# Kernel tuning notes

Measured on AMD Instinct MI355X. Metric: run time of the kernel, lower is better.

## Reference

```python
import jax, jax.numpy as jnp
import numpy as np
from jax.scipy.special import logsumexp

DIM_RHO = 128
DIM_C = 128
HID_F = 512   # hidden of MLP2 f
HID_F2 = 256  # hidden of MLP f2 (fixed 128->256->128 in source)
B, S, N = 64, 2048, 100000


def setup_inputs() -> dict:
    key = jax.random.key(0)
    ks = jax.random.split(key, 16)
    def lin(k, fan_in, fan_out):
        bound = 1.0 / np.sqrt(fan_in)
        kw, kb = jax.random.split(k)
        W = jax.random.uniform(kw, (fan_in, fan_out), jnp.float32, -bound, bound)
        b = jax.random.uniform(kb, (fan_out,), jnp.float32, -bound, bound)
        return W, b
    rho = jax.random.normal(ks[0], (B, S, DIM_RHO), jnp.float32)
    c = jax.random.normal(ks[1], (N, DIM_C), jnp.float32)
    w = jax.random.uniform(ks[2], (B, S), jnp.float32, 0.1, 1.0)
    l = jax.random.uniform(ks[3], (B,), jnp.float32, 0.1, 1.0)
    roads = jax.random.randint(ks[4], (B, S), 0, N + 1)  # 0 = pad row
    f2_W1, f2_b1 = lin(ks[5], DIM_C, HID_F2)
    f2_W2, f2_b2 = lin(ks[6], HID_F2, DIM_C)
    f_W1, f_b1 = lin(ks[7], DIM_RHO + DIM_C, HID_F)
    f_W21, f_b21 = lin(ks[8], HID_F, 1)
    f_W22, f_b22 = lin(ks[9], HID_F, 1)
    return {"rho": rho, "c": c, "w": w, "l": l, "roads": roads,
            "f2_W1": f2_W1, "f2_b1": f2_b1, "f2_W2": f2_W2, "f2_b2": f2_b2,
            "f_W1": f_W1, "f_b1": f_b1, "f_W21": f_W21, "f_b21": f_b21,
            "f_W22": f_W22, "f_b22": f_b22}


def reference(rho, c, w, l, roads, f2_W1, f2_b1, f2_W2, f2_b2,
              f_W1, f_b1, f_W21, f_b21, f_W22, f_b22):
    # pad row 0 with zeros, gather per-edge node features: (B, S, dim_c)
    c_padded = jnp.concatenate([jnp.zeros((1, c.shape[1]), c.dtype), c], axis=0)
    c_stack = c_padded[roads]
    # f2: MLP with SELU (dropout inactive at eval)
    h2 = jax.nn.selu(jnp.einsum('bsd,dh->bsh', c_stack, f2_W1) + f2_b1)
    c_t = jnp.einsum('bsh,hd->bsd', h2, f2_W2) + f2_b2
    # f: MLP2 with ReLU (use_selu=False), two heads
    x = jnp.concatenate([rho, c_t], axis=2)  # (B, S, 256)
    h1 = jax.nn.relu(jnp.einsum('bsd,dh->bsh', x, f_W1) + f_b1)
    logm = (jnp.einsum('bsh,ho->bso', h1, f_W21) + f_b21)[..., 0]  # (B, S)
    logv = (jnp.einsum('bsh,ho->bso', h1, f_W22) + f_b22)[..., 0]
    logw = jnp.log(w)
    logm_agg = logsumexp(logm + logw, axis=1)
    logv_agg = logsumexp(logv + 2.0 * logw, axis=1)
    logl = jnp.log(l)
    log_mu = logl - logm_agg
    log_lam = logl - 3.0 * logm_agg - logv_agg
    return (log_mu, log_lam)
```

## Files before the change

kernel.cpp:

```cpp
#include <hip/hip_runtime.h>
#include <hip/hip_bf16.h>

typedef __attribute__((ext_vector_type(8))) short short8;
typedef __attribute__((ext_vector_type(4))) float f32x4;

__device__ __forceinline__ unsigned short f2bf(float f){
    unsigned u = __float_as_uint(f);
    unsigned r = (u + 0x7FFFu + ((u >> 16) & 1u)) >> 16;
    return (unsigned short)r;
}

__device__ __forceinline__ unsigned swz(unsigned row, unsigned byte_in_row, unsigned stride){
    return row * stride + (byte_in_row ^ ((row & 15u) << 4));
}

__global__ void prep_weights(const float* __restrict__ W1, const float* __restrict__ W2,
                             const float* __restrict__ W3,
                             unsigned short* __restrict__ W1T,
                             unsigned short* __restrict__ W2T,
                             unsigned short* __restrict__ W3T){
    int i = blockIdx.x * 256 + threadIdx.x;
    if (i < 32768){
        int n = i >> 7, k = i & 127;
        W1T[i] = f2bf(W1[k * 256 + n]);
    } else if (i < 65536){
        int j = i - 32768; int n = j >> 8, k = j & 255;
        W2T[j] = f2bf(W2[k * 128 + n]);
    } else if (i < 196608){
        int j = i - 65536; int n = j >> 8, k = j & 255;
        W3T[j] = f2bf(W3[k * 512 + n]);
    }
}

__launch_bounds__(512, 2)
__global__ void main_kernel(const float* __restrict__ rho,
                            const float* __restrict__ c,
                            const float* __restrict__ w,
                            const int*  __restrict__ roads,
                            const unsigned short* __restrict__ W1T,
                            const float* __restrict__ b1,
                            const unsigned short* __restrict__ W2T,
                            const float* __restrict__ b2,
                            const unsigned short* __restrict__ W3T,
                            const float* __restrict__ b3,
                            const float* __restrict__ w21,
                            const float* __restrict__ b21s,
                            const float* __restrict__ w22,
                            const float* __restrict__ b22s,
                            float* __restrict__ pm,
                            float* __restrict__ pv)
{
    __shared__ __align__(16) unsigned char smem[65536];
    unsigned char* sXc  = smem;
    unsigned char* sH2  = smem + 16384;
    unsigned char* sRho = smem + 49152;
    float* sPm = (float*)(smem + 16384);
    float* sPv = (float*)(smem + 16384 + 2048);

    const int tid = threadIdx.x;
    const int t0  = blockIdx.x * 64;

    for (int u = tid; u < 64 * 32; u += 512){
        int row = u >> 5, ch = u & 31;
        int road = roads[t0 + row];
        float4 v = make_float4(0.f, 0.f, 0.f, 0.f);
        if (road > 0)
            v = reinterpret_cast<const float4*>(c + (size_t)(road - 1) * 128)[ch];
        ushort4 h;
        h.x = f2bf(v.x); h.y = f2bf(v.y); h.z = f2bf(v.z); h.w = f2bf(v.w);
        *reinterpret_cast<ushort4*>(sXc + swz(row, ch * 8, 256)) = h;

        float4 rv = reinterpret_cast<const float4*>(rho + (size_t)(t0 + row) * 128)[ch];
        ushort4 rh;
        rh.x = f2bf(rv.x); rh.y = f2bf(rv.y); rh.z = f2bf(rv.z); rh.w = f2bf(rv.w);
        *reinterpret_cast<ushort4*>(sRho + swz(row, ch * 8, 256)) = rh;
    }
    __syncthreads();

    const int lane = tid & 63, wv = tid >> 6;
    const int lr = lane & 15, lg = lane >> 4;

    #pragma unroll 1
    for (int nc = 0; nc < 2; ++nc){
        const int n0 = wv * 32 + nc * 16;
        short8 b[4];
        #pragma unroll
        for (int kk = 0; kk < 4; ++kk)
            b[kk] = *reinterpret_cast<const short8*>(W1T + (n0 + lr) * 128 + kk * 32 + lg * 8);
        f32x4 acc[4] = {{0.f,0.f,0.f,0.f},{0.f,0.f,0.f,0.f},{0.f,0.f,0.f,0.f},{0.f,0.f,0.f,0.f}};
        #pragma unroll
        for (int kk = 0; kk < 4; ++kk){
            #pragma unroll
            for (int mt = 0; mt < 4; ++mt){
                short8 a = *reinterpret_cast<const short8*>(sXc + swz(mt * 16 + lr, kk * 64 + lg * 16, 256));
                acc[mt] = __builtin_amdgcn_mfma_f32_16x16x32_bf16(b[kk], a, acc[mt], 0, 0, 0);
            }
        }
        float4 bb = *reinterpret_cast<const float4*>(b1 + n0 + lg * 4);
        #pragma unroll
        for (int mt = 0; mt < 4; ++mt){
            ushort4 h;
            #pragma unroll
            for (int r = 0; r < 4; ++r){
                float vv = acc[mt][r] + (&bb.x)[r];
                vv = (vv > 0.f) ? 1.0507009873554805f * vv
                                : 1.7580993408473766f * (__expf(vv) - 1.f);
                reinterpret_cast<unsigned short*>(&h)[r] = f2bf(vv);
            }
            *reinterpret_cast<ushort4*>(sH2 + swz(mt * 16 + lr, (n0 + lg * 4) * 2, 512)) = h;
        }
    }
    __syncthreads();

    {
        const int n0 = wv * 16;
        f32x4 acc[4] = {{0.f,0.f,0.f,0.f},{0.f,0.f,0.f,0.f},{0.f,0.f,0.f,0.f},{0.f,0.f,0.f,0.f}};
        #pragma unroll 1
        for (int h4 = 0; h4 < 2; ++h4){
            short8 b[4];
            #pragma unroll
            for (int kk = 0; kk < 4; ++kk)
                b[kk] = *reinterpret_cast<const short8*>(W2T + (n0 + lr) * 256 + (h4 * 4 + kk) * 32 + lg * 8);
            #pragma unroll
            for (int kk = 0; kk < 4; ++kk){
                #pragma unroll
                for (int mt = 0; mt < 4; ++mt){
                    short8 a = *reinterpret_cast<const short8*>(sH2 + swz(mt * 16 + lr, (h4 * 4 + kk) * 64 + lg * 16, 512));
                    acc[mt] = __builtin_amdgcn_mfma_f32_16x16x32_bf16(b[kk], a, acc[mt], 0, 0, 0);
                }
            }
        }
        float4 bb = *reinterpret_cast<const float4*>(b2 + n0 + lg * 4);
        #pragma unroll
        for (int mt = 0; mt < 4; ++mt){
            ushort4 h;
            #pragma unroll
            for (int r = 0; r < 4; ++r){
                float vv = acc[mt][r] + (&bb.x)[r];
                reinterpret_cast<unsigned short*>(&h)[r] = f2bf(vv);
            }
            *reinterpret_cast<ushort4*>(sXc + swz(mt * 16 + lr, (n0 + lg * 4) * 2, 256)) = h;
        }
    }
    __syncthreads();

    float hm[4] = {0.f, 0.f, 0.f, 0.f};
    float hv[4] = {0.f, 0.f, 0.f, 0.f};
    #pragma unroll 1
    for (int nc = 0; nc < 4; ++nc){
        const int n0 = wv * 64 + nc * 16;
        f32x4 acc[4] = {{0.f,0.f,0.f,0.f},{0.f,0.f,0.f,0.f},{0.f,0.f,0.f,0.f},{0.f,0.f,0.f,0.f}};
        #pragma unroll 1
        for (int h4 = 0; h4 < 2; ++h4){
            const unsigned char* src = h4 ? sXc : sRho;
            short8 b[4];
            #pragma unroll
            for (int kk = 0; kk < 4; ++kk)
                b[kk] = *reinterpret_cast<const short8*>(W3T + (n0 + lr) * 256 + (h4 * 4 + kk) * 32 + lg * 8);
            #pragma unroll
            for (int kk = 0; kk < 4; ++kk){
                #pragma unroll
                for (int mt = 0; mt < 4; ++mt){
                    short8 a = *reinterpret_cast<const short8*>(src + swz(mt * 16 + lr, kk * 64 + lg * 16, 256));
                    acc[mt] = __builtin_amdgcn_mfma_f32_16x16x32_bf16(b[kk], a, acc[mt], 0, 0, 0);
                }
            }
        }
        float4 b3q = *reinterpret_cast<const float4*>(b3  + n0 + lg * 4);
        float4 wmq = *reinterpret_cast<const float4*>(w21 + n0 + lg * 4);
        float4 wvq = *reinterpret_cast<const float4*>(w22 + n0 + lg * 4);
        #pragma unroll
        for (int mt = 0; mt < 4; ++mt){
            #pragma unroll
            for (int r = 0; r < 4; ++r){
                float h = fmaxf(acc[mt][r] + (&b3q.x)[r], 0.f);
                hm[mt] += h * (&wmq.x)[r];
                hv[mt] += h * (&wvq.x)[r];
            }
        }
    }
    #pragma unroll
    for (int mt = 0; mt < 4; ++mt){
        hm[mt] += __shfl_xor(hm[mt], 16, 64);
        hm[mt] += __shfl_xor(hm[mt], 32, 64);
        hv[mt] += __shfl_xor(hv[mt], 16, 64);
        hv[mt] += __shfl_xor(hv[mt], 32, 64);
    }
    if (lg == 0){
        #pragma unroll
        for (int mt = 0; mt < 4; ++mt){
            sPm[wv * 64 + mt * 16 + lr] = hm[mt];
            sPv[wv * 64 + mt * 16 + lr] = hv[mt];
        }
    }
    __syncthreads();
    if (tid < 64){
        float B21 = b21s[0], B22 = b22s[0];
        float m_ = B21, v_ = B22;
        #pragma unroll
        for (int k = 0; k < 8; ++k){
            m_ += sPm[k * 64 + tid];
            v_ += sPv[k * 64 + tid];
        }
        int t = t0 + tid;
        float lw = logf(w[t]);
        pm[t] = m_ + lw;
        pv[t] = v_ + 2.f * lw;
    }
}

__global__ void reduce_kernel(const float* __restrict__ pm, const float* __restrict__ pv,
                              const float* __restrict__ l, float* __restrict__ out){
    int b = blockIdx.x;
    int tid = threadIdx.x;
    const float* Pm = pm + (size_t)b * 2048;
    const float* Pv = pv + (size_t)b * 2048;

    float mm = -1e30f, mv = -1e30f;
    for (int i = tid; i < 2048; i += 256){
        mm = fmaxf(mm, Pm[i]);
        mv = fmaxf(mv, Pv[i]);
    }
    __shared__ float redm[4], redv[4];
    #pragma unroll
    for (int off = 32; off > 0; off >>= 1){
        mm = fmaxf(mm, __shfl_xor(mm, off, 64));
        mv = fmaxf(mv, __shfl_xor(mv, off, 64));
    }
    int wv = tid >> 6;
    if ((tid & 63) == 0){ redm[wv] = mm; redv[wv] = mv; }
    __syncthreads();
    mm = fmaxf(fmaxf(redm[0], redm[1]), fmaxf(redm[2], redm[3]));
    mv = fmaxf(fmaxf(redv[0], redv[1]), fmaxf(redv[2], redv[3]));

    float sm = 0.f, sv = 0.f;
    for (int i = tid; i < 2048; i += 256){
        sm += expf(Pm[i] - mm);
        sv += expf(Pv[i] - mv);
    }
    #pragma unroll
    for (int off = 32; off > 0; off >>= 1){
        sm += __shfl_xor(sm, off, 64);
        sv += __shfl_xor(sv, off, 64);
    }
    __shared__ float red2m[4], red2v[4];
    if ((tid & 63) == 0){ red2m[wv] = sm; red2v[wv] = sv; }
    __syncthreads();
    if (tid == 0){
        sm = red2m[0] + red2m[1] + red2m[2] + red2m[3];
        sv = red2v[0] + red2v[1] + red2v[2] + red2v[3];
        float lsem = mm + logf(sm);
        float lsev = mv + logf(sv);
        float ll = logf(l[b]);
        out[b]      = ll - lsem;
        out[64 + b] = ll - 3.f * lsem - lsev;
    }
}

extern "C" void kernel_launch(void* const* d_in, const int* in_sizes, int n_in,
                              void* d_out, int out_size, void* d_ws, size_t ws_size,
                              hipStream_t stream){
    const float* rho   = (const float*)d_in[0];
    const float* c     = (const float*)d_in[1];
    const float* w     = (const float*)d_in[2];
    const float* l     = (const float*)d_in[3];
    const int*   roads = (const int*)  d_in[4];
    const float* f2_W1 = (const float*)d_in[5];
    const float* f2_b1 = (const float*)d_in[6];
    const float* f2_W2 = (const float*)d_in[7];
    const float* f2_b2 = (const float*)d_in[8];
    const float* f_W1  = (const float*)d_in[9];
    const float* f_b1  = (const float*)d_in[10];
    const float* f_W21 = (const float*)d_in[11];
    const float* f_b21 = (const float*)d_in[12];
    const float* f_W22 = (const float*)d_in[13];
    const float* f_b22 = (const float*)d_in[14];

    unsigned char* ws = (unsigned char*)d_ws;
    unsigned short* W1T = (unsigned short*)(ws);
    unsigned short* W2T = (unsigned short*)(ws + 65536);
    unsigned short* W3T = (unsigned short*)(ws + 131072);
    float* pm = (float*)(ws + 393216);
    float* pv = (float*)(ws + 393216 + 524288);

    prep_weights<<<768, 256, 0, stream>>>(f2_W1, f2_W2, f_W1, W1T, W2T, W3T);
    main_kernel<<<2048, 512, 0, stream>>>(rho, c, w, roads,
                                          W1T, f2_b1, W2T, f2_b2, W3T, f_b1,
                                          f_W21, f_b21, f_W22, f_b22, pm, pv);
    reduce_kernel<<<64, 256, 0, stream>>>(pm, pv, l, (float*)d_out);
}
```

Before: 129.1 us.

## Restructure MFMA loops to reuse LDS A-fragments across multiple output tiles

The three GEMM stages are reorganised so each wave loads its LDS A-fragments once per k-step and applies them to several weight tiles (2 or 4 N-tiles) held in registers, instead of reloading the A tile for every N chunk. The second GEMM is also repartitioned so each wave owns one 16-row M tile and 64 output columns rather than all rows and 16 columns. This targets LDS read traffic and gives more independent MFMAs between loads, at the cost of more accumulator registers, which may lower occupancy.

```diff
diff --git a/kernel.cpp b/kernel.cpp
--- a/kernel.cpp
+++ b/kernel.cpp
@@ -80,66 +80,68 @@
     const int lane = tid & 63, wv = tid >> 6;
     const int lr = lane & 15, lg = lane >> 4;
 
-    #pragma unroll 1
-    for (int nc = 0; nc < 2; ++nc){
-        const int n0 = wv * 32 + nc * 16;
-        short8 b[4];
-        #pragma unroll
-        for (int kk = 0; kk < 4; ++kk)
-            b[kk] = *reinterpret_cast<const short8*>(W1T + (n0 + lr) * 128 + kk * 32 + lg * 8);
-        f32x4 acc[4] = {{0.f,0.f,0.f,0.f},{0.f,0.f,0.f,0.f},{0.f,0.f,0.f,0.f},{0.f,0.f,0.f,0.f}};
+    {
+        f32x4 acc[2][4] = {};
         #pragma unroll
         for (int kk = 0; kk < 4; ++kk){
+            short8 a[4], b[2];
+            #pragma unroll
+            for (int mt = 0; mt < 4; ++mt)
+                a[mt] = *reinterpret_cast<const short8*>(sXc + swz(mt * 16 + lr, kk * 64 + lg * 16, 256));
+            #pragma unroll
+            for (int nc = 0; nc < 2; ++nc)
+                b[nc] = *reinterpret_cast<const short8*>(W1T + (wv * 32 + nc * 16 + lr) * 128 + kk * 32 + lg * 8);
+            #pragma unroll
+            for (int nc = 0; nc < 2; ++nc)
+                #pragma unroll
+                for (int mt = 0; mt < 4; ++mt)
+                    acc[nc][mt] = __builtin_amdgcn_mfma_f32_16x16x32_bf16(b[nc], a[mt], acc[nc][mt], 0, 0, 0);
+        }
+        #pragma unroll
+        for (int nc = 0; nc < 2; ++nc){
+            const int n0 = wv * 32 + nc * 16;
+            float4 bb = *reinterpret_cast<const float4*>(b1 + n0 + lg * 4);
             #pragma unroll
             for (int mt = 0; mt < 4; ++mt){
-                short8 a = *reinterpret_cast<const short8*>(sXc + swz(mt * 16 + lr, kk * 64 + lg * 16, 256));
-                acc[mt] = __builtin_amdgcn_mfma_f32_16x16x32_bf16(b[kk], a, acc[mt], 0, 0, 0);
+                ushort4 h;
+                #pragma unroll
+                for (int r = 0; r < 4; ++r){
+                    float vv = acc[nc][mt][r] + (&bb.x)[r];
+                    vv = (vv > 0.f) ? 1.0507009873554805f * vv
+                                    : 1.7580993408473766f * (__expf(vv) - 1.f);
+                    reinterpret_cast<unsigned short*>(&h)[r] = f2bf(vv);
+                }
+                *reinterpret_cast<ushort4*>(sH2 + swz(mt * 16 + lr, (n0 + lg * 4) * 2, 512)) = h;
             }
         }
-        float4 bb = *reinterpret_cast<const float4*>(b1 + n0 + lg * 4);
-        #pragma unroll
-        for (int mt = 0; mt < 4; ++mt){
+    }
+    __syncthreads();
+
+    {
+        const int mt2 = wv >> 1, nh = wv & 1;
+        f32x4 acc[4] = {};
+        #pragma unroll
+        for (int kk = 0; kk < 8; ++kk){
+            short8 a = *reinterpret_cast<const short8*>(sH2 + swz(mt2 * 16 + lr, kk * 64 + lg * 16, 512));
+            short8 b[4];
+            #pragma unroll
+            for (int nc = 0; nc < 4; ++nc)
+                b[nc] = *reinterpret_cast<const short8*>(W2T + (nh * 64 + nc * 16 + lr) * 256 + kk * 32 + lg * 8);
+            #pragma unroll
+            for (int nc = 0; nc < 4; ++nc)
+                acc[nc] = __builtin_amdgcn_mfma_f32_16x16x32_bf16(b[nc], a, acc[nc], 0, 0, 0);
+        }
+        #pragma unroll
+        for (int nc = 0; nc < 4; ++nc){
+            const int n0 = nh * 64 + nc * 16;
+            float4 bb = *reinterpret_cast<const float4*>(b2 + n0 + lg * 4);
             ushort4 h;
             #pragma unroll
             for (int r = 0; r < 4; ++r){
-                float vv = acc[mt][r] + (&bb.x)[r];
-                vv = (vv > 0.f) ? 1.0507009873554805f * vv
-                                : 1.7580993408473766f * (__expf(vv) - 1.f);
+                float vv = acc[nc][r] + (&bb.x)[r];
                 reinterpret_cast<unsigned short*>(&h)[r] = f2bf(vv);
             }
-            *reinterpret_cast<ushort4*>(sH2 + swz(mt * 16 + lr, (n0 + lg * 4) * 2, 512)) = h;
-        }
-    }
-    __syncthreads();
-
-    {
-        const int n0 = wv * 16;
-        f32x4 acc[4] = {{0.f,0.f,0.f,0.f},{0.f,0.f,0.f,0.f},{0.f,0.f,0.f,0.f},{0.f,0.f,0.f,0.f}};
-        #pragma unroll 1
-        for (int h4 = 0; h4 < 2; ++h4){
-            short8 b[4];
-            #pragma unroll
-            for (int kk = 0; kk < 4; ++kk)
-                b[kk] = *reinterpret_cast<const short8*>(W2T + (n0 + lr) * 256 + (h4 * 4 + kk) * 32 + lg * 8);
-            #pragma unroll
-            for (int kk = 0; kk < 4; ++kk){
-                #pragma unroll
-                for (int mt = 0; mt < 4; ++mt){
-                    short8 a = *reinterpret_cast<const short8*>(sH2 + swz(mt * 16 + lr, (h4 * 4 + kk) * 64 + lg * 16, 512));
-                    acc[mt] = __builtin_amdgcn_mfma_f32_16x16x32_bf16(b[kk], a, acc[mt], 0, 0, 0);
-                }
-            }
-        }
-        float4 bb = *reinterpret_cast<const float4*>(b2 + n0 + lg * 4);
-        #pragma unroll
-        for (int mt = 0; mt < 4; ++mt){
-            ushort4 h;
-            #pragma unroll
-            for (int r = 0; r < 4; ++r){
-                float vv = acc[mt][r] + (&bb.x)[r];
-                reinterpret_cast<unsigned short*>(&h)[r] = f2bf(vv);
-            }
-            *reinterpret_cast<ushort4*>(sXc + swz(mt * 16 + lr, (n0 + lg * 4) * 2, 256)) = h;
+            *reinterpret_cast<ushort4*>(sXc + swz(mt2 * 16 + lr, (n0 + lg * 4) * 2, 256)) = h;
         }
     }
     __syncthreads();
@@ -147,35 +149,52 @@
     float hm[4] = {0.f, 0.f, 0.f, 0.f};
     float hv[4] = {0.f, 0.f, 0.f, 0.f};
     #pragma unroll 1
-    for (int nc = 0; nc < 4; ++nc){
-        const int n0 = wv * 64 + nc * 16;
-        f32x4 acc[4] = {{0.f,0.f,0.f,0.f},{0.f,0.f,0.f,0.f},{0.f,0.f,0.f,0.f},{0.f,0.f,0.f,0.f}};
-        #pragma unroll 1
-        for (int h4 = 0; h4 < 2; ++h4){
-            const unsigned char* src = h4 ? sXc : sRho;
-            short8 b[4];
-            #pragma unroll
-            for (int kk = 0; kk < 4; ++kk)
-                b[kk] = *reinterpret_cast<const short8*>(W3T + (n0 + lr) * 256 + (h4 * 4 + kk) * 32 + lg * 8);
-            #pragma unroll
-            for (int kk = 0; kk < 4; ++kk){
-                #pragma unroll
-                for (int mt = 0; mt < 4; ++mt){
-                    short8 a = *reinterpret_cast<const short8*>(src + swz(mt * 16 + lr, kk * 64 + lg * 16, 256));
-                    acc[mt] = __builtin_amdgcn_mfma_f32_16x16x32_bf16(b[kk], a, acc[mt], 0, 0, 0);
+    for (int h = 0; h < 2; ++h){
+        f32x4 acc[2][4] = {};
+        #pragma unroll
+        for (int kk = 0; kk < 4; ++kk){
+            short8 a[4], b[2];
+            #pragma unroll
+            for (int mt = 0; mt < 4; ++mt)
+                a[mt] = *reinterpret_cast<const short8*>(sRho + swz(mt * 16 + lr, kk * 64 + lg * 16, 256));
+            #pragma unroll
+            for (int j = 0; j < 2; ++j)
+                b[j] = *reinterpret_cast<const short8*>(W3T + (wv * 64 + (h * 2 + j) * 16 + lr) * 256 + kk * 32 + lg * 8);
+            #pragma unroll
+            for (int j = 0; j < 2; ++j)
+                #pragma unroll
+                for (int mt = 0; mt < 4; ++mt)
+                    acc[j][mt] = __builtin_amdgcn_mfma_f32_16x16x32_bf16(b[j], a[mt], acc[j][mt], 0, 0, 0);
+        }
+        #pragma unroll
+        for (int kk = 0; kk < 4; ++kk){
+            short8 a[4], b[2];
+            #pragma unroll
+            for (int mt = 0; mt < 4; ++mt)
+                a[mt] = *reinterpret_cast<const short8*>(sXc + swz(mt * 16 + lr, kk * 64 + lg * 16, 256));
+            #pragma unroll
+            for (int j = 0; j < 2; ++j)
+                b[j] = *reinterpret_cast<const short8*>(W3T + (wv * 64 + (h * 2 + j) * 16 + lr) * 256 + (4 + kk) * 32 + lg * 8);
+            #pragma unroll
+            for (int j = 0; j < 2; ++j)
+                #pragma unroll
+                for (int mt = 0; mt < 4; ++mt)
+                    acc[j][mt] = __builtin_amdgcn_mfma_f32_16x16x32_bf16(b[j], a[mt], acc[j][mt], 0, 0, 0);
+        }
+        #pragma unroll
+        for (int j = 0; j < 2; ++j){
+            const int n0 = wv * 64 + (h * 2 + j) * 16;
+            float4 b3q = *reinterpret_cast<const float4*>(b3  + n0 + lg * 4);
+            float4 wmq = *reinterpret_cast<const float4*>(w21 + n0 + lg * 4);
+            float4 wvq = *reinterpret_cast<const float4*>(w22 + n0 + lg * 4);
+            #pragma unroll
+            for (int mt = 0; mt < 4; ++mt){
+                #pragma unroll
+                for (int r = 0; r < 4; ++r){
+                    float hh = fmaxf(acc[j][mt][r] + (&b3q.x)[r], 0.f);
+                    hm[mt] += hh * (&wmq.x)[r];
+                    hv[mt] += hh * (&wvq.x)[r];
                 }
-            }
-        }
-        float4 b3q = *reinterpret_cast<const float4*>(b3  + n0 + lg * 4);
-        float4 wmq = *reinterpret_cast<const float4*>(w21 + n0 + lg * 4);
-        float4 wvq = *reinterpret_cast<const float4*>(w22 + n0 + lg * 4);
-        #pragma unroll
-        for (int mt = 0; mt < 4; ++mt){
-            #pragma unroll
-            for (int r = 0; r < 4; ++r){
-                float h = fmaxf(acc[mt][r] + (&b3q.x)[r], 0.f);
-                hm[mt] += h * (&wmq.x)[r];
-                hv[mt] += h * (&wvq.x)[r];
             }
         }
     }
```

Measured after the change: 201.4 us. 1.56x slower.

## Split f2 hidden layer into halves to cut LDS and raise occupancy

Applied to the files above, without the earlier changes.

Computes the 256-wide SELU hidden layer of f2 in two 128-column halves, consuming each half straight into the second GEMM's accumulators. The 32KB hidden buffer shrinks to 16KB, cutting shared memory per block from 64KB to 48KB, and launch bounds go from 2 to 3 blocks per CU. The second GEMM is re-partitioned so each wave owns one 16-row m-tile and 64 output columns. In exchange it adds two extra block barriers and tighter register limits, which could cause spills.

```diff
diff --git a/kernel.cpp b/kernel.cpp
--- a/kernel.cpp
+++ b/kernel.cpp
@@ -32,7 +32,7 @@
     }
 }
 
-__launch_bounds__(512, 2)
+__launch_bounds__(512, 3)
 __global__ void main_kernel(const float* __restrict__ rho,
                             const float* __restrict__ c,
                             const float* __restrict__ w,
@@ -50,10 +50,10 @@
                             float* __restrict__ pm,
                             float* __restrict__ pv)
 {
-    __shared__ __align__(16) unsigned char smem[65536];
-    unsigned char* sXc  = smem;
-    unsigned char* sH2  = smem + 16384;
-    unsigned char* sRho = smem + 49152;
+    __shared__ __align__(16) unsigned char smem[49152];
+    unsigned char* sXc   = smem;
+    unsigned char* sHalf = smem + 16384;
+    unsigned char* sRho  = smem + 32768;
     float* sPm = (float*)(smem + 16384);
     float* sPv = (float*)(smem + 16384 + 2048);
 
@@ -79,67 +79,68 @@
 
     const int lane = tid & 63, wv = tid >> 6;
     const int lr = lane & 15, lg = lane >> 4;
+    const int mt2 = wv >> 1, nh = wv & 1;
+
+    f32x4 acc2[4] = {};
 
     #pragma unroll 1
-    for (int nc = 0; nc < 2; ++nc){
-        const int n0 = wv * 32 + nc * 16;
-        short8 b[4];
-        #pragma unroll
-        for (int kk = 0; kk < 4; ++kk)
-            b[kk] = *reinterpret_cast<const short8*>(W1T + (n0 + lr) * 128 + kk * 32 + lg * 8);
-        f32x4 acc[4] = {{0.f,0.f,0.f,0.f},{0.f,0.f,0.f,0.f},{0.f,0.f,0.f,0.f},{0.f,0.f,0.f,0.f}};
-        #pragma unroll
-        for (int kk = 0; kk < 4; ++kk){
+    for (int p = 0; p < 2; ++p){
+        {
+            const int n0 = p * 128 + wv * 16;
+            f32x4 acc[4] = {};
+            #pragma unroll
+            for (int kk = 0; kk < 4; ++kk){
+                short8 b = *reinterpret_cast<const short8*>(W1T + (n0 + lr) * 128 + kk * 32 + lg * 8);
+                #pragma unroll
+                for (int mt = 0; mt < 4; ++mt){
+                    short8 a = *reinterpret_cast<const short8*>(sXc + swz(mt * 16 + lr, kk * 64 + lg * 16, 256));
+                    acc[mt] = __builtin_amdgcn_mfma_f32_16x16x32_bf16(b, a, acc[mt], 0, 0, 0);
+                }
+            }
+            float4 bb = *reinterpret_cast<const float4*>(b1 + n0 + lg * 4);
             #pragma unroll
             for (int mt = 0; mt < 4; ++mt){
-                short8 a = *reinterpret_cast<const short8*>(sXc + swz(mt * 16 + lr, kk * 64 + lg * 16, 256));
-                acc[mt] = __builtin_amdgcn_mfma_f32_16x16x32_bf16(b[kk], a, acc[mt], 0, 0, 0);
-            }
-        }
-        float4 bb = *reinterpret_cast<const float4*>(b1 + n0 + lg * 4);
-        #pragma unroll
-        for (int mt = 0; mt < 4; ++mt){
+                ushort4 h;
+                #pragma unroll
+                for (int r = 0; r < 4; ++r){
+                    float vv = acc[mt][r] + (&bb.x)[r];
+                    vv = (vv > 0.f) ? 1.0507009873554805f * vv
+                                    : 1.7580993408473766f * (__expf(vv) - 1.f);
+                    reinterpret_cast<unsigned short*>(&h)[r] = f2bf(vv);
+                }
+                *reinterpret_cast<ushort4*>(sHalf + swz(mt * 16 + lr, (wv * 16 + lg * 4) * 2, 256)) = h;
+            }
+        }
+        __syncthreads();
+
+        {
+            #pragma unroll
+            for (int kk = 0; kk < 4; ++kk){
+                short8 a = *reinterpret_cast<const short8*>(sHalf + swz(mt2 * 16 + lr, kk * 64 + lg * 16, 256));
+                short8 b[4];
+                #pragma unroll
+                for (int nc = 0; nc < 4; ++nc)
+                    b[nc] = *reinterpret_cast<const short8*>(W2T + (nh * 64 + nc * 16 + lr) * 256 + (p * 4 + kk) * 32 + lg * 8);
+                #pragma unroll
+                for (int nc = 0; nc < 4; ++nc)
+                    acc2[nc] = __builtin_amdgcn_mfma_f32_16x16x32_bf16(b[nc], a, acc2[nc], 0, 0, 0);
+            }
+        }
+        __syncthreads();
+    }
+
+    {
+        #pragma unroll
+        for (int nc = 0; nc < 4; ++nc){
+            const int n0 = nh * 64 + nc * 16;
+            float4 bb = *reinterpret_cast<const float4*>(b2 + n0 + lg * 4);
             ushort4 h;
             #pragma unroll
             for (int r = 0; r < 4; ++r){
-                float vv = acc[mt][r] + (&bb.x)[r];
-                vv = (vv > 0.f) ? 1.0507009873554805f * vv
-                                : 1.7580993408473766f * (__expf(vv) - 1.f);
+                float vv = acc2[nc][r] + (&bb.x)[r];
                 reinterpret_cast<unsigned short*>(&h)[r] = f2bf(vv);
             }
-            *reinterpret_cast<ushort4*>(sH2 + swz(mt * 16 + lr, (n0 + lg * 4) * 2, 512)) = h;
-        }
-    }
-    __syncthreads();
-
-    {
-        const int n0 = wv * 16;
-        f32x4 acc[4] = {{0.f,0.f,0.f,0.f},{0.f,0.f,0.f,0.f},{0.f,0.f,0.f,0.f},{0.f,0.f,0.f,0.f}};
-        #pragma unroll 1
-        for (int h4 = 0; h4 < 2; ++h4){
-            short8 b[4];
-            #pragma unroll
-            for (int kk = 0; kk < 4; ++kk)
-                b[kk] = *reinterpret_cast<const short8*>(W2T + (n0 + lr) * 256 + (h4 * 4 + kk) * 32 + lg * 8);
-            #pragma unroll
-            for (int kk = 0; kk < 4; ++kk){
-                #pragma unroll
-                for (int mt = 0; mt < 4; ++mt){
-                    short8 a = *reinterpret_cast<const short8*>(sH2 + swz(mt * 16 + lr, (h4 * 4 + kk) * 64 + lg * 16, 512));
-                    acc[mt] = __builtin_amdgcn_mfma_f32_16x16x32_bf16(b[kk], a, acc[mt], 0, 0, 0);
-                }
-            }
-        }
-        float4 bb = *reinterpret_cast<const float4*>(b2 + n0 + lg * 4);
-        #pragma unroll
-        for (int mt = 0; mt < 4; ++mt){
-            ushort4 h;
-            #pragma unroll
-            for (int r = 0; r < 4; ++r){
-                float vv = acc[mt][r] + (&bb.x)[r];
-                reinterpret_cast<unsigned short*>(&h)[r] = f2bf(vv);
-            }
-            *reinterpret_cast<ushort4*>(sXc + swz(mt * 16 + lr, (n0 + lg * 4) * 2, 256)) = h;
+            *reinterpret_cast<ushort4*>(sXc + swz(mt2 * 16 + lr, (n0 + lg * 4) * 2, 256)) = h;
         }
     }
     __syncthreads();
@@ -149,7 +150,7 @@
     #pragma unroll 1
     for (int nc = 0; nc < 4; ++nc){
         const int n0 = wv * 64 + nc * 16;
-        f32x4 acc[4] = {{0.f,0.f,0.f,0.f},{0.f,0.f,0.f,0.f},{0.f,0.f,0.f,0.f},{0.f,0.f,0.f,0.f}};
+        f32x4 acc[4] = {};
         #pragma unroll 1
         for (int h4 = 0; h4 < 2; ++h4){
             const unsigned char* src = h4 ? sXc : sRho;
```

Result: slower. 176.6 us (+36.8%).

## Loop four 64-row tiles per block and repartition second GEMM across waves

Applied to the files above, without the earlier changes.

The main kernel now runs 512 blocks, each looping over four 64-row tiles instead of one tile per block, which cuts block launch count. The second MLP layer is repartitioned so each wave handles one 16-row m-tile and 64 output columns, loading weight fragments inline. This reduces per-block setup, but gather, compute and store phases are still serialized with barriers inside each tile, and the grid may not fill all CUs as well. An extra barrier is added at the end of each tile, and an unused weight-load loop is left in.

```diff
diff --git a/kernel.cpp b/kernel.cpp
--- a/kernel.cpp
+++ b/kernel.cpp
@@ -58,154 +58,164 @@
     float* sPv = (float*)(smem + 16384 + 2048);
 
     const int tid = threadIdx.x;
-    const int t0  = blockIdx.x * 64;
-
-    for (int u = tid; u < 64 * 32; u += 512){
-        int row = u >> 5, ch = u & 31;
-        int road = roads[t0 + row];
-        float4 v = make_float4(0.f, 0.f, 0.f, 0.f);
-        if (road > 0)
-            v = reinterpret_cast<const float4*>(c + (size_t)(road - 1) * 128)[ch];
-        ushort4 h;
-        h.x = f2bf(v.x); h.y = f2bf(v.y); h.z = f2bf(v.z); h.w = f2bf(v.w);
-        *reinterpret_cast<ushort4*>(sXc + swz(row, ch * 8, 256)) = h;
-
-        float4 rv = reinterpret_cast<const float4*>(rho + (size_t)(t0 + row) * 128)[ch];
-        ushort4 rh;
-        rh.x = f2bf(rv.x); rh.y = f2bf(rv.y); rh.z = f2bf(rv.z); rh.w = f2bf(rv.w);
-        *reinterpret_cast<ushort4*>(sRho + swz(row, ch * 8, 256)) = rh;
-    }
-    __syncthreads();
-
     const int lane = tid & 63, wv = tid >> 6;
     const int lr = lane & 15, lg = lane >> 4;
+    const int mt2 = wv >> 1, nh = wv & 1;
 
     #pragma unroll 1
-    for (int nc = 0; nc < 2; ++nc){
-        const int n0 = wv * 32 + nc * 16;
-        short8 b[4];
-        #pragma unroll
-        for (int kk = 0; kk < 4; ++kk)
-            b[kk] = *reinterpret_cast<const short8*>(W1T + (n0 + lr) * 128 + kk * 32 + lg * 8);
-        f32x4 acc[4] = {{0.f,0.f,0.f,0.f},{0.f,0.f,0.f,0.f},{0.f,0.f,0.f,0.f},{0.f,0.f,0.f,0.f}};
-        #pragma unroll
-        for (int kk = 0; kk < 4; ++kk){
+    for (int tile = 0; tile < 4; ++tile){
+        const int t0 = (blockIdx.x * 4 + tile) * 64;
+
+        for (int u = tid; u < 64 * 32; u += 512){
+            int row = u >> 5, ch = u & 31;
+            int road = roads[t0 + row];
+            float4 v = make_float4(0.f, 0.f, 0.f, 0.f);
+            if (road > 0)
+                v = reinterpret_cast<const float4*>(c + (size_t)(road - 1) * 128)[ch];
+            ushort4 h;
+            h.x = f2bf(v.x); h.y = f2bf(v.y); h.z = f2bf(v.z); h.w = f2bf(v.w);
+            *reinterpret_cast<ushort4*>(sXc + swz(row, ch * 8, 256)) = h;
+
+            float4 rv = reinterpret_cast<const float4*>(rho + (size_t)(t0 + row) * 128)[ch];
+            ushort4 rh;
+            rh.x = f2bf(rv.x); rh.y = f2bf(rv.y); rh.z = f2bf(rv.z); rh.w = f2bf(rv.w);
+            *reinterpret_cast<ushort4*>(sRho + swz(row, ch * 8, 256)) = rh;
+        }
+        __syncthreads();
+
+        #pragma unroll 1
+        for (int nc = 0; nc < 2; ++nc){
+            const int n0 = wv * 32 + nc * 16;
+            short8 b[4];
+            #pragma unroll
+            for (int kk = 0; kk < 4; ++kk)
+                b[kk] = *reinterpret_cast<const short8*>(W1T + (n0 + lr) * 128 + kk * 32 + lg * 8);
+            f32x4 acc[4] = {};
+            #pragma unroll
+            for (int kk = 0; kk < 4; ++kk){
+                #pragma unroll
+                for (int mt = 0; mt < 4; ++mt){
+                    short8 a = *reinterpret_cast<const short8*>(sXc + swz(mt * 16 + lr, kk * 64 + lg * 16, 256));
+                    acc[mt] = __builtin_amdgcn_mfma_f32_16x16x32_bf16(b[kk], a, acc[mt], 0, 0, 0);
+                }
+            }
+            float4 bb = *reinterpret_cast<const float4*>(b1 + n0 + lg * 4);
             #pragma unroll
             for (int mt = 0; mt < 4; ++mt){
-                short8 a = *reinterpret_cast<const short8*>(sXc + swz(mt * 16 + lr, kk * 64 + lg * 16, 256));
-                acc[mt] = __builtin_amdgcn_mfma_f32_16x16x32_bf16(b[kk], a, acc[mt], 0, 0, 0);
-            }
-        }
-        float4 bb = *reinterpret_cast<const float4*>(b1 + n0 + lg * 4);
+                ushort4 h;
+                #pragma unroll
+                for (int r = 0; r < 4; ++r){
+                    float vv = acc[mt][r] + (&bb.x)[r];
+                    vv = (vv > 0.f) ? 1.0507009873554805f * vv
+                                    : 1.7580993408473766f * (__expf(vv) - 1.f);
+                    reinterpret_cast<unsigned short*>(&h)[r] = f2bf(vv);
+                }
+                *reinterpret_cast<ushort4*>(sH2 + swz(mt * 16 + lr, (n0 + lg * 4) * 2, 512)) = h;
+            }
+        }
+        __syncthreads();
+
+        {
+            f32x4 acc[4] = {};
+            #pragma unroll 1
+            for (int h4 = 0; h4 < 2; ++h4){
+                short8 b[4];
+                #pragma unroll
+                for (int kk = 0; kk < 4; ++kk)
+                    b[kk] = *reinterpret_cast<const short8*>(W2T + (nh * 64 + (kk & 3) * 16 + lr) * 256 + 0);
+                #pragma unroll
+                for (int kk = 0; kk < 4; ++kk){
+                    short8 a = *reinterpret_cast<const short8*>(sH2 + swz(mt2 * 16 + lr, (h4 * 4 + kk) * 64 + lg * 16, 512));
+                    short8 bb0 = *reinterpret_cast<const short8*>(W2T + (nh * 64 +  0 + lr) * 256 + (h4 * 4 + kk) * 32 + lg * 8);
+                    short8 bb1 = *reinterpret_cast<const short8*>(W2T + (nh * 64 + 16 + lr) * 256 + (h4 * 4 + kk) * 32 + lg * 8);
+                    short8 bb2 = *reinterpret_cast<const short8*>(W2T + (nh * 64 + 32 + lr) * 256 + (h4 * 4 + kk) * 32 + lg * 8);
+                    short8 bb3 = *reinterpret_cast<const short8*>(W2T + (nh * 64 + 48 + lr) * 256 + (h4 * 4 + kk) * 32 + lg * 8);
+                    acc[0] = __builtin_amdgcn_mfma_f32_16x16x32_bf16(bb0, a, acc[0], 0, 0, 0);
+                    acc[1] = __builtin_amdgcn_mfma_f32_16x16x32_bf16(bb1, a, acc[1], 0, 0, 0);
+                    acc[2] = __builtin_amdgcn_mfma_f32_16x16x32_bf16(bb2, a, acc[2], 0, 0, 0);
+                    acc[3] = __builtin_amdgcn_mfma_f32_16x16x32_bf16(bb3, a, acc[3], 0, 0, 0);
+                }
+                (void)b;
+            }
+            #pragma unroll
+            for (int nc = 0; nc < 4; ++nc){
+                const int n0 = nh * 64 + nc * 16;
+                float4 bb = *reinterpret_cast<const float4*>(b2 + n0 + lg * 4);
+                ushort4 h;
+                #pragma unroll
+                for (int r = 0; r < 4; ++r){
+                    float vv = acc[nc][r] + (&bb.x)[r];
+                    reinterpret_cast<unsigned short*>(&h)[r] = f2bf(vv);
+                }
+                *reinterpret_cast<ushort4*>(sXc + swz(mt2 * 16 + lr, (n0 + lg * 4) * 2, 256)) = h;
+            }
+        }
+        __syncthreads();
+
+        float hm[4] = {0.f, 0.f, 0.f, 0.f};
+        float hv[4] = {0.f, 0.f, 0.f, 0.f};
+        #pragma unroll 1
+        for (int nc = 0; nc < 4; ++nc){
+            const int n0 = wv * 64 + nc * 16;
+            f32x4 acc[4] = {};
+            #pragma unroll 1
+            for (int h4 = 0; h4 < 2; ++h4){
+                const unsigned char* src = h4 ? sXc : sRho;
+                short8 b[4];
+                #pragma unroll
+                for (int kk = 0; kk < 4; ++kk)
+                    b[kk] = *reinterpret_cast<const short8*>(W3T + (n0 + lr) * 256 + (h4 * 4 + kk) * 32 + lg * 8);
+                #pragma unroll
+                for (int kk = 0; kk < 4; ++kk){
+                    #pragma unroll
+                    for (int mt = 0; mt < 4; ++mt){
+                        short8 a = *reinterpret_cast<const short8*>(src + swz(mt * 16 + lr, kk * 64 + lg * 16, 256));
+                        acc[mt] = __builtin_amdgcn_mfma_f32_16x16x32_bf16(b[kk], a, acc[mt], 0, 0, 0);
+                    }
+                }
+            }
+            float4 b3q = *reinterpret_cast<const float4*>(b3  + n0 + lg * 4);
+            float4 wmq = *reinterpret_cast<const float4*>(w21 + n0 + lg * 4);
+            float4 wvq = *reinterpret_cast<const float4*>(w22 + n0 + lg * 4);
+            #pragma unroll
+            for (int mt = 0; mt < 4; ++mt){
+                #pragma unroll
+                for (int r = 0; r < 4; ++r){
+                    float h = fmaxf(acc[mt][r] + (&b3q.x)[r], 0.f);
+                    hm[mt] += h * (&wmq.x)[r];
+                    hv[mt] += h * (&wvq.x)[r];
+                }
+            }
+        }
         #pragma unroll
         for (int mt = 0; mt < 4; ++mt){
-            ushort4 h;
-            #pragma unroll
-            for (int r = 0; r < 4; ++r){
-                float vv = acc[mt][r] + (&bb.x)[r];
-                vv = (vv > 0.f) ? 1.0507009873554805f * vv
-                                : 1.7580993408473766f * (__expf(vv) - 1.f);
-                reinterpret_cast<unsigned short*>(&h)[r] = f2bf(vv);
-            }
-            *reinterpret_cast<ushort4*>(sH2 + swz(mt * 16 + lr, (n0 + lg * 4) * 2, 512)) = h;
-        }
-    }
-    __syncthreads();
-
-    {
-        const int n0 = wv * 16;
-        f32x4 acc[4] = {{0.f,0.f,0.f,0.f},{0.f,0.f,0.f,0.f},{0.f,0.f,0.f,0.f},{0.f,0.f,0.f,0.f}};
-        #pragma unroll 1
-        for (int h4 = 0; h4 < 2; ++h4){
-            short8 b[4];
-            #pragma unroll
-            for (int kk = 0; kk < 4; ++kk)
-                b[kk] = *reinterpret_cast<const short8*>(W2T + (n0 + lr) * 256 + (h4 * 4 + kk) * 32 + lg * 8);
-            #pragma unroll
-            for (int kk = 0; kk < 4; ++kk){
-                #pragma unroll
-                for (int mt = 0; mt < 4; ++mt){
-                    short8 a = *reinterpret_cast<const short8*>(sH2 + swz(mt * 16 + lr, (h4 * 4 + kk) * 64 + lg * 16, 512));
-                    acc[mt] = __builtin_amdgcn_mfma_f32_16x16x32_bf16(b[kk], a, acc[mt], 0, 0, 0);
-                }
-            }
-        }
-        float4 bb = *reinterpret_cast<const float4*>(b2 + n0 + lg * 4);
-        #pragma unroll
-        for (int mt = 0; mt < 4; ++mt){
-            ushort4 h;
-            #pragma unroll
-            for (int r = 0; r < 4; ++r){
-                float vv = acc[mt][r] + (&bb.x)[r];
-                reinterpret_cast<unsigned short*>(&h)[r] = f2bf(vv);
-            }
-            *reinterpret_cast<ushort4*>(sXc + swz(mt * 16 + lr, (n0 + lg * 4) * 2, 256)) = h;
-        }
-    }
-    __syncthreads();
-
-    float hm[4] = {0.f, 0.f, 0.f, 0.f};
-    float hv[4] = {0.f, 0.f, 0.f, 0.f};
-    #pragma unroll 1
-    for (int nc = 0; nc < 4; ++nc){
-        const int n0 = wv * 64 + nc * 16;
-        f32x4 acc[4] = {{0.f,0.f,0.f,0.f},{0.f,0.f,0.f,0.f},{0.f,0.f,0.f,0.f},{0.f,0.f,0.f,0.f}};
-        #pragma unroll 1
-        for (int h4 = 0; h4 < 2; ++h4){
-            const unsigned char* src = h4 ? sXc : sRho;
-            short8 b[4];
-            #pragma unroll
-            for (int kk = 0; kk < 4; ++kk)
-                b[kk] = *reinterpret_cast<const short8*>(W3T + (n0 + lr) * 256 + (h4 * 4 + kk) * 32 + lg * 8);
-            #pragma unroll
-            for (int kk = 0; kk < 4; ++kk){
-                #pragma unroll
-                for (int mt = 0; mt < 4; ++mt){
-                    short8 a = *reinterpret_cast<const short8*>(src + swz(mt * 16 + lr, kk * 64 + lg * 16, 256));
-                    acc[mt] = __builtin_amdgcn_mfma_f32_16x16x32_bf16(b[kk], a, acc[mt], 0, 0, 0);
-                }
-            }
-        }
-        float4 b3q = *reinterpret_cast<const float4*>(b3  + n0 + lg * 4);
-        float4 wmq = *reinterpret_cast<const float4*>(w21 + n0 + lg * 4);
-        float4 wvq = *reinterpret_cast<const float4*>(w22 + n0 + lg * 4);
-        #pragma unroll
-        for (int mt = 0; mt < 4; ++mt){
-            #pragma unroll
-            for (int r = 0; r < 4; ++r){
-                float h = fmaxf(acc[mt][r] + (&b3q.x)[r], 0.f);
-                hm[mt] += h * (&wmq.x)[r];
-                hv[mt] += h * (&wvq.x)[r];
-            }
-        }
-    }
-    #pragma unroll
-    for (int mt = 0; mt < 4; ++mt){
-        hm[mt] += __shfl_xor(hm[mt], 16, 64);
-        hm[mt] += __shfl_xor(hm[mt], 32, 64);
-        hv[mt] += __shfl_xor(hv[mt], 16, 64);
-        hv[mt] += __shfl_xor(hv[mt], 32, 64);
-    }
-    if (lg == 0){
-        #pragma unroll
-        for (int mt = 0; mt < 4; ++mt){
-            sPm[wv * 64 + mt * 16 + lr] = hm[mt];
-            sPv[wv * 64 + mt * 16 + lr] = hv[mt];
-        }
-    }
-    __syncthreads();
-    if (tid < 64){
-        float B21 = b21s[0], B22 = b22s[0];
-        float m_ = B21, v_ = B22;
-        #pragma unroll
-        for (int k = 0; k < 8; ++k){
-            m_ += sPm[k * 64 + tid];
-            v_ += sPv[k * 64 + tid];
-        }
-        int t = t0 + tid;
-        float lw = logf(w[t]);
-        pm[t] = m_ + lw;
-        pv[t] = v_ + 2.f * lw;
+            hm[mt] += __shfl_xor(hm[mt], 16, 64);
+            hm[mt] += __shfl_xor(hm[mt], 32, 64);
+            hv[mt] += __shfl_xor(hv[mt], 16, 64);
+            hv[mt] += __shfl_xor(hv[mt], 32, 64);
+        }
+        if (lg == 0){
+            #pragma unroll
+            for (int mt = 0; mt < 4; ++mt){
+                sPm[wv * 64 + mt * 16 + lr] = hm[mt];
+                sPv[wv * 64 + mt * 16 + lr] = hv[mt];
+            }
+        }
+        __syncthreads();
+        if (tid < 64){
+            float B21 = b21s[0], B22 = b22s[0];
+            float m_ = B21, v_ = B22;
+            #pragma unroll
+            for (int k = 0; k < 8; ++k){
+                m_ += sPm[k * 64 + tid];
+                v_ += sPv[k * 64 + tid];
+            }
+            int t = t0 + tid;
+            float lw = logf(w[t]);
+            pm[t] = m_ + lw;
+            pv[t] = v_ + 2.f * lw;
+        }
+        __syncthreads();
     }
 }
 
@@ -284,8 +294,8 @@
     float* pv = (float*)(ws + 393216 + 524288);
 
     prep_weights<<<768, 256, 0, stream>>>(f2_W1, f2_W2, f_W1, W1T, W2T, W3T);
-    main_kernel<<<2048, 512, 0, stream>>>(rho, c, w, roads,
-                                          W1T, f2_b1, W2T, f2_b2, W3T, f_b1,
-                                          f_W21, f_b21, f_W22, f_b22, pm, pv);
+    main_kernel<<<512, 512, 0, stream>>>(rho, c, w, roads,
+                                         W1T, f2_b1, W2T, f2_b2, W3T, f_b1,
+                                         f_W21, f_b21, f_W22, f_b22, pm, pv);
     reduce_kernel<<<64, 256, 0, stream>>>(pm, pv, l, (float*)d_out);
 }
```

Measured after the change: 196.5 us. 1.52x slower.
